# Optimization experiments

Hardware: AMD Instinct MI355X
Metric: run time of the kernel (lower is better)

Reference implementation:

```python
import jax, jax.numpy as jnp
import numpy as np

N_NODES = 50000
N_EDGES = 800000
IN_CH = 128
HID = 64
HEADS = 4
OUT_CH = 12
NEG_SLOPE = 0.2


def setup_inputs() -> dict:
    key = jax.random.key(0)
    ks = jax.random.split(key, 16)
    s = 0.05
    F1 = HEADS * HID  # 256
    return {
        "x": jax.random.normal(ks[0], (N_NODES, IN_CH), jnp.float32),
        "edge_index": jax.random.randint(ks[1], (2, N_EDGES), 0, N_NODES, jnp.int64 if jax.config.jax_enable_x64 else jnp.int32),
        # GAT layer 1 params
        "W1": jax.random.normal(ks[2], (IN_CH, F1), jnp.float32) * s,
        "att_src1": jax.random.normal(ks[3], (HEADS, HID), jnp.float32) * s,
        "att_dst1": jax.random.normal(ks[4], (HEADS, HID), jnp.float32) * s,
        "b1": jnp.zeros((F1,), jnp.float32),
        # GAT layer 2 params
        "W2": jax.random.normal(ks[5], (F1, F1), jnp.float32) * s,
        "att_src2": jax.random.normal(ks[6], (HEADS, HID), jnp.float32) * s,
        "att_dst2": jax.random.normal(ks[7], (HEADS, HID), jnp.float32) * s,
        "b2": jnp.zeros((F1,), jnp.float32),
        # temporal Conv1d(F1 -> HID, k=3, pad=1)
        "conv_w": jax.random.normal(ks[8], (HID, F1, 3), jnp.float32) * s,
        "conv_b": jnp.zeros((HID,), jnp.float32),
        # final Linear(HID -> OUT_CH)
        "lin_w": jax.random.normal(ks[9], (HID, OUT_CH), jnp.float32) * s,
        "lin_b": jnp.zeros((OUT_CH,), jnp.float32),
    }


def _gat_layer(x, src, dst, W, a_src, a_dst, bias):
    # x: [N, Fin]; src/dst: [E] (self-loops already included)
    h = (x @ W).reshape(x.shape[0], HEADS, HID)          # [N, H, C]
    alpha_s = jnp.sum(h * a_src[None], axis=-1)          # [N, H]
    alpha_d = jnp.sum(h * a_dst[None], axis=-1)          # [N, H]
    e = jax.nn.leaky_relu(alpha_s[src] + alpha_d[dst], NEG_SLOPE)  # [E, H]
    # segment softmax over destination nodes
    m = jax.ops.segment_max(e, dst, num_segments=N_NODES)          # [N, H]
    ex = jnp.exp(e - m[dst])
    denom = jax.ops.segment_sum(ex, dst, num_segments=N_NODES)
    alpha = ex / (denom[dst] + 1e-16)                    # [E, H]
    msg = h[src] * alpha[:, :, None]                     # [E, H, C]
    out = jax.ops.segment_sum(msg, dst, num_segments=N_NODES)      # [N, H, C]
    return out.reshape(N_NODES, HEADS * HID) + bias


def reference(x, edge_index, W1, att_src1, att_dst1, b1, W2, att_src2, att_dst2, b2, conv_w, conv_b, lin_w, lin_b):
    # add self loops (PyG GATConv default)
    loops = jnp.arange(N_NODES, dtype=edge_index.dtype)
    src = jnp.concatenate([edge_index[0], loops])
    dst = jnp.concatenate([edge_index[1], loops])

    h = jax.nn.relu(_gat_layer(x, src, dst, W1, att_src1, att_dst1, b1))
    h = jax.nn.relu(_gat_layer(h, src, dst, W2, att_src2, att_dst2, b2))

    # temporal Conv1d over the node axis: [1, F1, N] -> [1, HID, N]
    inp = h.T[None]                                      # [1, F1, N]
    y = jax.lax.conv_general_dilated(inp, conv_w, (1,), [(1, 1)],
                                     dimension_numbers=("NCH", "OIH", "NCH"))
    y = jax.nn.relu(y + conv_b[None, :, None])           # [1, HID, N]
    out = y[0].T @ lin_w + lin_b                         # [N, OUT_CH]
    return out
```

## Files before the change

### kernel.cpp

```cpp
#include <hip/hip_runtime.h>
#include <hip/hip_bf16.h>

#define N_NODES 50000
#define N_EDGES 800000
#define E_TOT   (N_EDGES + N_NODES)
#define IN_CH   128
#define HID     64
#define HEADS   4
#define F1      256
#define OUT_CH  12
#define NEG_SLOPE 0.2f
#define CAP     256

typedef __attribute__((ext_vector_type(8))) short  bf16x8;
typedef __attribute__((ext_vector_type(4))) float  f32x4;

__device__ __forceinline__ float leaky(float x) { return x > 0.f ? x : NEG_SLOPE * x; }

__device__ __forceinline__ unsigned short tob(float f) {
    unsigned u = __float_as_uint(f);
    u += 0x7fffu + ((u >> 16) & 1u);
    return (unsigned short)(u >> 16);
}
__device__ __forceinline__ float fromb(unsigned short s) {
    return __uint_as_float(((unsigned)s) << 16);
}

typedef __attribute__((address_space(3))) unsigned int        lds_u32;
typedef const __attribute__((address_space(1))) unsigned int  glb_u32;
__device__ __forceinline__ void gload16(const void* g, void* l) {
    __builtin_amdgcn_global_load_lds((glb_u32*)g, (lds_u32*)l, 16, 0, 0);
}

__global__ void k_zero(int* p, int n) {
    int i = blockIdx.x * blockDim.x + threadIdx.x;
    if (i < n) p[i] = 0;
}

__global__ void k_guard(unsigned int* front, unsigned int* back) {
    int i = threadIdx.x;
    if (i < 128) front[i] = 0;
    else         back[i - 128] = 0;
}

__global__ void k_count(const int* __restrict__ ei, int* __restrict__ counts) {
    int i = blockIdx.x * blockDim.x + threadIdx.x;
    if (i >= E_TOT) return;
    int dst = (i < N_EDGES) ? ei[N_EDGES + i] : (i - N_EDGES);
    atomicAdd(&counts[dst], 1);
}

__global__ __launch_bounds__(1024) void k_scan(const int* __restrict__ counts,
                                               int* __restrict__ rowptr,
                                               int* __restrict__ cursor) {
    __shared__ int wsum[16];
    __shared__ int carrysh;
    const int lane = threadIdx.x & 63, w = threadIdx.x >> 6;
    if (threadIdx.x == 0) carrysh = 0;
    __syncthreads();
    for (int base = 0; base < N_NODES; base += 1024) {
        int i = base + threadIdx.x;
        int v = (i < N_NODES) ? counts[i] : 0;
        int s = v;
        #pragma unroll
        for (int off = 1; off < 64; off <<= 1) {
            int t = __shfl_up(s, off);
            if (lane >= off) s += t;
        }
        if (lane == 63) wsum[w] = s;
        __syncthreads();
        int woff = 0;
        for (int j = 0; j < w; ++j) woff += wsum[j];
        int incl = carrysh + woff + s;
        if (i < N_NODES) { rowptr[i] = incl - v; cursor[i] = incl - v; }
        __syncthreads();
        if (threadIdx.x == 1023) carrysh = incl;
        __syncthreads();
    }
    if (threadIdx.x == 0) rowptr[N_NODES] = carrysh;
}

__global__ void k_fill(const int* __restrict__ ei, int* __restrict__ cursor,
                       int* __restrict__ csr_src) {
    int i = blockIdx.x * blockDim.x + threadIdx.x;
    if (i >= E_TOT) return;
    int src, dst;
    if (i < N_EDGES) { src = ei[i]; dst = ei[N_EDGES + i]; }
    else             { src = dst = i - N_EDGES; }
    int pos = atomicAdd(&cursor[dst], 1);
    csr_src[pos] = src;
}

__global__ void k_cast4(const float* __restrict__ in, unsigned short* __restrict__ out, int n4) {
    int i = blockIdx.x * blockDim.x + threadIdx.x;
    if (i >= n4) return;
    float4 v = *(const float4*)&in[i * 4];
    ushort4 o;
    o.x = tob(v.x); o.y = tob(v.y); o.z = tob(v.z); o.w = tob(v.w);
    *(ushort4*)&out[i * 4] = o;
}

__global__ void k_prep_wt(const float* __restrict__ W, unsigned short* __restrict__ WT,
                          int K, int N) {
    int idx = blockIdx.x * blockDim.x + threadIdx.x;
    if (idx >= K * N) return;
    int n = idx / K, k = idx % K;
    WT[idx] = tob(W[(size_t)k * N + n]);
}

__global__ void k_prep_cw(const float* __restrict__ CW, unsigned short* __restrict__ BT) {
    int idx = blockIdx.x * blockDim.x + threadIdx.x;
    if (idx >= 64 * 768) return;
    int o = idx / 768, kk = idx % 768;
    int kseg = kk >> 8, c = kk & 255;
    BT[idx] = tob(CW[((size_t)o * 256 + c) * 3 + kseg]);
}

__global__ __launch_bounds__(256) void k_gemm_bf16(const unsigned short* __restrict__ A,
                                                   const unsigned short* __restrict__ BT,
                                                   unsigned short* __restrict__ C,
                                                   int M, int K) {
    __shared__ unsigned short As[128][32];
    __shared__ unsigned short Bs[128][32];
    const int t    = threadIdx.x;
    const int lane = t & 63, wave = t >> 6;
    const int wr = wave >> 1, wc = wave & 1;
    const int row0 = blockIdx.y * 128, col0 = blockIdx.x * 128;
    const int l15 = lane & 15, kg = lane >> 4;

    const int srow = (wave << 4) + (lane >> 2);
    const int sseg = (lane & 3) * 8;
    int ar0 = row0 + srow;      if (ar0 >= M) ar0 = M - 1;
    int ar1 = row0 + srow + 64; if (ar1 >= M) ar1 = M - 1;
    const int br0 = col0 + srow, br1 = col0 + srow + 64;
    unsigned short* ldsA = &As[0][0];
    unsigned short* ldsB = &Bs[0][0];
    const int lofs0 = wave * 512, lofs1 = 2048 + wave * 512;

    f32x4 acc[4][4];
    #pragma unroll
    for (int m = 0; m < 4; ++m)
        #pragma unroll
        for (int n = 0; n < 4; ++n) acc[m][n] = 0.f;

    for (int k0 = 0; k0 < K; k0 += 32) {
        gload16(&A [(size_t)ar0 * K + k0 + sseg], ldsA + lofs0);
        gload16(&A [(size_t)ar1 * K + k0 + sseg], ldsA + lofs1);
        gload16(&BT[(size_t)br0 * K + k0 + sseg], ldsB + lofs0);
        gload16(&BT[(size_t)br1 * K + k0 + sseg], ldsB + lofs1);
        __syncthreads();
        bf16x8 af[4], bf[4];
        #pragma unroll
        for (int m = 0; m < 4; ++m) af[m] = *(const bf16x8*)&As[wr * 64 + m * 16 + l15][kg * 8];
        #pragma unroll
        for (int n = 0; n < 4; ++n) bf[n] = *(const bf16x8*)&Bs[wc * 64 + n * 16 + l15][kg * 8];
        #pragma unroll
        for (int m = 0; m < 4; ++m)
            #pragma unroll
            for (int n = 0; n < 4; ++n)
                acc[m][n] = __builtin_amdgcn_mfma_f32_16x16x32_bf16(af[m], bf[n], acc[m][n], 0, 0, 0);
        __syncthreads();
    }
    #pragma unroll
    for (int m = 0; m < 4; ++m) {
        #pragma unroll
        for (int j = 0; j < 4; ++j) {
            int row = row0 + wr * 64 + m * 16 + (lane >> 4) * 4 + j;
            if (row < M) {
                #pragma unroll
                for (int n = 0; n < 4; ++n)
                    C[(size_t)row * F1 + col0 + wc * 64 + n * 16 + l15] = tob(acc[m][n][j]);
            }
        }
    }
}

__global__ __launch_bounds__(256) void k_attn(const unsigned short* __restrict__ H,
                                              const float* __restrict__ a_src,
                                              const float* __restrict__ a_dst,
                                              float* __restrict__ oS,
                                              float* __restrict__ oD) {
    int lane = threadIdx.x & 63, wid = threadIdx.x >> 6;
    int node = blockIdx.x * 4 + wid;
    int head = lane >> 4, cc = (lane & 15) * 4;
    ushort4 hv4 = *(const ushort4*)&H[(size_t)node * F1 + lane * 4];
    float h0 = fromb(hv4.x), h1 = fromb(hv4.y), h2 = fromb(hv4.z), h3 = fromb(hv4.w);
    float4 sv = *(const float4*)&a_src[head * HID + cc];
    float4 dv = *(const float4*)&a_dst[head * HID + cc];
    float s = h0 * sv.x + h1 * sv.y + h2 * sv.z + h3 * sv.w;
    float d = h0 * dv.x + h1 * dv.y + h2 * dv.z + h3 * dv.w;
    #pragma unroll
    for (int off = 1; off < 16; off <<= 1) {
        s += __shfl_xor(s, off);
        d += __shfl_xor(d, off);
    }
    if ((lane & 15) == 0) { oS[node * 4 + head] = s; oD[node * 4 + head] = d; }
}

__global__ __launch_bounds__(256) void k_agg(const unsigned short* __restrict__ H,
                                             const float* __restrict__ aS,
                                             const float* __restrict__ aD,
                                             const int* __restrict__ rowptr,
                                             const int* __restrict__ csr,
                                             const float* __restrict__ bias,
                                             unsigned short* __restrict__ O) {
    __shared__ float wlds[4][CAP][4];
    int lane = threadIdx.x & 63, wid = threadIdx.x >> 6;
    int node = blockIdx.x * 4 + wid;
    int beg = rowptr[node], end = rowptr[node + 1];
    int deg = end - beg;

    float4 adv = *(const float4*)&aD[node * 4];
    float ad[4] = { adv.x, adv.y, adv.z, adv.w };
    float m[4] = { -1e30f, -1e30f, -1e30f, -1e30f };

    for (int j = beg + lane, idx = lane; j < end; j += 64, idx += 64) {
        int src = csr[j];
        float4 asv = *(const float4*)&aS[src * 4];
        float4 e4;
        e4.x = leaky(asv.x + ad[0]);
        e4.y = leaky(asv.y + ad[1]);
        e4.z = leaky(asv.z + ad[2]);
        e4.w = leaky(asv.w + ad[3]);
        m[0] = fmaxf(m[0], e4.x); m[1] = fmaxf(m[1], e4.y);
        m[2] = fmaxf(m[2], e4.z); m[3] = fmaxf(m[3], e4.w);
        if (idx < CAP) *(float4*)&wlds[wid][idx][0] = e4;
    }
    #pragma unroll
    for (int off = 1; off < 64; off <<= 1) {
        #pragma unroll
        for (int h = 0; h < 4; ++h) m[h] = fmaxf(m[h], __shfl_xor(m[h], off));
    }

    float s[4] = { 0.f, 0.f, 0.f, 0.f };
    int degc = deg < CAP ? deg : CAP;
    for (int idx = lane; idx < degc; idx += 64) {
        float4 e4 = *(float4*)&wlds[wid][idx][0];
        float4 w4;
        w4.x = __expf(e4.x - m[0]); w4.y = __expf(e4.y - m[1]);
        w4.z = __expf(e4.z - m[2]); w4.w = __expf(e4.w - m[3]);
        s[0] += w4.x; s[1] += w4.y; s[2] += w4.z; s[3] += w4.w;
        *(float4*)&wlds[wid][idx][0] = w4;
    }
    for (int j = beg + CAP + lane; j < end; j += 64) {
        int src = csr[j];
        float4 asv = *(const float4*)&aS[src * 4];
        s[0] += __expf(leaky(asv.x + ad[0]) - m[0]);
        s[1] += __expf(leaky(asv.y + ad[1]) - m[1]);
        s[2] += __expf(leaky(asv.z + ad[2]) - m[2]);
        s[3] += __expf(leaky(asv.w + ad[3]) - m[3]);
    }
    #pragma unroll
    for (int off = 1; off < 64; off <<= 1) {
        #pragma unroll
        for (int h = 0; h < 4; ++h) s[h] += __shfl_xor(s[h], off);
    }

    int   hl   = lane >> 4;
    float invh = 1.f / (s[hl] + 1e-16f);
    float mh   = m[hl];
    float adh  = ad[hl];
    float a0 = 0.f, a1 = 0.f, a2 = 0.f, a3 = 0.f;
    for (int idx = 0; idx < degc; ++idx) {
        int src = csr[beg + idx];
        float w = wlds[wid][idx][hl];
        ushort4 hv = *(const ushort4*)&H[(size_t)src * F1 + lane * 4];
        a0 += w * fromb(hv.x); a1 += w * fromb(hv.y);
        a2 += w * fromb(hv.z); a3 += w * fromb(hv.w);
    }
    for (int idx = CAP; idx < deg; ++idx) {
        int src = csr[beg + idx];
        float w = __expf(leaky(aS[src * 4 + hl] + adh) - mh);
        ushort4 hv = *(const ushort4*)&H[(size_t)src * F1 + lane * 4];
        a0 += w * fromb(hv.x); a1 += w * fromb(hv.y);
        a2 += w * fromb(hv.z); a3 += w * fromb(hv.w);
    }
    float4 bv = *(const float4*)&bias[lane * 4];
    ushort4 o;
    o.x = tob(fmaxf(a0 * invh + bv.x, 0.f));
    o.y = tob(fmaxf(a1 * invh + bv.y, 0.f));
    o.z = tob(fmaxf(a2 * invh + bv.z, 0.f));
    o.w = tob(fmaxf(a3 * invh + bv.w, 0.f));
    *(ushort4*)&O[(size_t)node * F1 + lane * 4] = o;
}

__global__ __launch_bounds__(256) void k_conv(const unsigned short* __restrict__ H,
                                              const unsigned short* __restrict__ BcT,
                                              const float* __restrict__ CB,
                                              float* __restrict__ Y) {
    __shared__ unsigned short As[128][32];
    __shared__ unsigned short Bs[64][32];
    const int t    = threadIdx.x;
    const int lane = t & 63, wave = t >> 6;
    const int row0 = blockIdx.x * 128;
    const int l15 = lane & 15, kg = lane >> 4;

    const int srow = (wave << 4) + (lane >> 2);
    const int sseg = (lane & 3) * 8;
    unsigned short* ldsA = &As[0][0];
    unsigned short* ldsB = &Bs[0][0];
    const int lofs0 = wave * 512, lofs1 = 2048 + wave * 512;

    f32x4 acc[2][4];
    #pragma unroll
    for (int m = 0; m < 2; ++m)
        #pragma unroll
        for (int n = 0; n < 4; ++n) acc[m][n] = 0.f;

    for (int k0 = 0; k0 < 768; k0 += 32) {
        int kseg  = k0 >> 8;
        int cbase = (k0 & 255) + sseg;
        int gr0 = row0 + srow + kseg - 1;
        int gr1 = gr0 + 64;
        if (gr1 > N_NODES) gr1 = N_NODES;
        gload16(H + (ptrdiff_t)gr0 * F1 + cbase, ldsA + lofs0);
        gload16(H + (ptrdiff_t)gr1 * F1 + cbase, ldsA + lofs1);
        {
            int brow = srow;
            gload16(&BcT[(size_t)brow * 768 + k0 + sseg], ldsB + lofs0);
        }
        __syncthreads();
        bf16x8 af[2], bf[4];
        #pragma unroll
        for (int m = 0; m < 2; ++m) af[m] = *(const bf16x8*)&As[wave * 32 + m * 16 + l15][kg * 8];
        #pragma unroll
        for (int n = 0; n < 4; ++n) bf[n] = *(const bf16x8*)&Bs[n * 16 + l15][kg * 8];
        #pragma unroll
        for (int m = 0; m < 2; ++m)
            #pragma unroll
            for (int n = 0; n < 4; ++n)
                acc[m][n] = __builtin_amdgcn_mfma_f32_16x16x32_bf16(af[m], bf[n], acc[m][n], 0, 0, 0);
        __syncthreads();
    }
    #pragma unroll
    for (int m = 0; m < 2; ++m) {
        #pragma unroll
        for (int j = 0; j < 4; ++j) {
            int row = row0 + wave * 32 + m * 16 + (lane >> 4) * 4 + j;
            if (row < N_NODES) {
                #pragma unroll
                for (int n = 0; n < 4; ++n) {
                    int col = n * 16 + l15;
                    Y[(size_t)row * HID + col] = fmaxf(acc[m][n][j] + CB[col], 0.f);
                }
            }
        }
    }
}

__global__ __launch_bounds__(256) void k_lin(const float* __restrict__ Y,
                                             const float* __restrict__ LW,
                                             const float* __restrict__ LB,
                                             float* __restrict__ OUT) {
    __shared__ float w[64][12];
    __shared__ float b[12];
    for (int i = threadIdx.x; i < 64 * 12; i += 256) w[i / 12][i % 12] = LW[i];
    if (threadIdx.x < 12) b[threadIdx.x] = LB[threadIdx.x];
    __syncthreads();
    int n = blockIdx.x * 256 + threadIdx.x;
    if (n >= N_NODES) return;
    float acc[12];
    #pragma unroll
    for (int o = 0; o < 12; ++o) acc[o] = b[o];
    for (int c = 0; c < 64; c += 4) {
        float4 yv = *(const float4*)&Y[(size_t)n * HID + c];
        #pragma unroll
        for (int o = 0; o < 12; ++o)
            acc[o] += yv.x * w[c][o] + yv.y * w[c + 1][o]
                    + yv.z * w[c + 2][o] + yv.w * w[c + 3][o];
    }
    #pragma unroll
    for (int o = 0; o < 12; ++o) OUT[(size_t)n * OUT_CH + o] = acc[o];
}

extern "C" void kernel_launch(void* const* d_in, const int* in_sizes, int n_in,
                              void* d_out, int out_size, void* d_ws, size_t ws_size,
                              hipStream_t stream) {
    const float* x   = (const float*)d_in[0];
    const int*   ei  = (const int*)d_in[1];
    const float* W1  = (const float*)d_in[2];
    const float* as1 = (const float*)d_in[3];
    const float* ad1 = (const float*)d_in[4];
    const float* b1  = (const float*)d_in[5];
    const float* W2  = (const float*)d_in[6];
    const float* as2 = (const float*)d_in[7];
    const float* ad2 = (const float*)d_in[8];
    const float* b2  = (const float*)d_in[9];
    const float* cw  = (const float*)d_in[10];
    const float* cb  = (const float*)d_in[11];
    const float* lw  = (const float*)d_in[12];
    const float* lb  = (const float*)d_in[13];
    float* out = (float*)d_out;

    char* ws = (char*)d_ws;
    size_t off = 0;
    auto alloc = [&](size_t bytes) -> void* {
        off = (off + 255) & ~(size_t)255;
        void* p = ws + off;
        off += bytes;
        return p;
    };
    unsigned short* hA  = (unsigned short*)alloc((size_t)N_NODES * F1 * 2);
    unsigned short* hBg = (unsigned short*)alloc((size_t)(N_NODES + 2) * F1 * 2);
    unsigned short* hB  = hBg + F1;
    unsigned short* xb  = (unsigned short*)alloc((size_t)N_NODES * IN_CH * 2);
    unsigned short* wt1 = (unsigned short*)alloc((size_t)F1 * IN_CH * 2);
    unsigned short* wt2 = (unsigned short*)alloc((size_t)F1 * F1 * 2);
    unsigned short* cwt = (unsigned short*)alloc((size_t)HID * 768 * 2);
    float* alS    = (float*)alloc((size_t)N_NODES * 4 * 4);
    float* alD    = (float*)alloc((size_t)N_NODES * 4 * 4);
    int*   counts = (int*)  alloc((size_t)N_NODES * 4);
    int*   rowptr = (int*)  alloc((size_t)(N_NODES + 1) * 4);
    int*   cursor = (int*)  alloc((size_t)N_NODES * 4);
    int*   csr    = (int*)  alloc((size_t)E_TOT * 4);
    float* y      = (float*)alloc((size_t)N_NODES * HID * 4);

    k_zero <<<(N_NODES + 255) / 256, 256, 0, stream>>>(counts, N_NODES);
    k_guard<<<1, 256, 0, stream>>>((unsigned int*)hBg,
                                   (unsigned int*)(hBg + (size_t)(N_NODES + 1) * F1));
    k_count<<<(E_TOT + 255) / 256, 256, 0, stream>>>(ei, counts);
    k_scan <<<1, 1024, 0, stream>>>(counts, rowptr, cursor);
    k_fill <<<(E_TOT + 255) / 256, 256, 0, stream>>>(ei, cursor, csr);

    k_cast4 <<<(N_NODES * IN_CH / 4 + 255) / 256, 256, 0, stream>>>(x, xb, N_NODES * IN_CH / 4);
    k_prep_wt<<<(IN_CH * F1 + 255) / 256, 256, 0, stream>>>(W1, wt1, IN_CH, F1);
    k_prep_wt<<<(F1 * F1 + 255) / 256, 256, 0, stream>>>(W2, wt2, F1, F1);
    k_prep_cw<<<(HID * 768 + 255) / 256, 256, 0, stream>>>(cw, cwt);

    dim3 gg(F1 / 128, (N_NODES + 127) / 128);
    k_gemm_bf16<<<gg, 256, 0, stream>>>(xb, wt1, hA, N_NODES, IN_CH);
    k_attn<<<N_NODES / 4, 256, 0, stream>>>(hA, as1, ad1, alS, alD);
    k_agg <<<N_NODES / 4, 256, 0, stream>>>(hA, alS, alD, rowptr, csr, b1, hB);
    k_gemm_bf16<<<gg, 256, 0, stream>>>(hB, wt2, hA, N_NODES, F1);
    k_attn<<<N_NODES / 4, 256, 0, stream>>>(hA, as2, ad2, alS, alD);
    k_agg <<<N_NODES / 4, 256, 0, stream>>>(hA, alS, alD, rowptr, csr, b2, hB);
    k_conv<<<(N_NODES + 127) / 128, 256, 0, stream>>>(hB, cwt, cb, y);
    k_lin <<<(N_NODES + 255) / 256, 256, 0, stream>>>(y, lw, lb, out);
}
```

Measured before the change: 468.9 us.

## Split GAT aggregation across four edge groups per wave with wide loads

The per-node aggregation used to have all 64 lanes walk every edge serially, each lane holding 4 features. Now the wave is split into four groups of 16 lanes. Each group processes every fourth edge and each lane loads 16 bf16 features with two 128-bit loads. Partial sums are combined with cross-group shuffles and only group 0 writes the output. This raises memory-level parallelism and shortens the serial edge loop, at the cost of more registers, 32 shuffles and idle lanes during the write.

```diff
diff --git a/kernel.cpp b/kernel.cpp
--- a/kernel.cpp
+++ b/kernel.cpp
@@ -256,32 +256,53 @@
         for (int h = 0; h < 4; ++h) s[h] += __shfl_xor(s[h], off);
     }
 
-    int   hl   = lane >> 4;
-    float invh = 1.f / (s[hl] + 1e-16f);
-    float mh   = m[hl];
-    float adh  = ad[hl];
-    float a0 = 0.f, a1 = 0.f, a2 = 0.f, a3 = 0.f;
-    for (int idx = 0; idx < degc; ++idx) {
+    const int g   = lane >> 4;
+    const int l15 = lane & 15;
+    const int hl  = l15 >> 2;
+    float acc[16];
+    #pragma unroll
+    for (int k = 0; k < 16; ++k) acc[k] = 0.f;
+
+    for (int idx = g; idx < degc; idx += 4) {
         int src = csr[beg + idx];
         float w = wlds[wid][idx][hl];
-        ushort4 hv = *(const ushort4*)&H[(size_t)src * F1 + lane * 4];
-        a0 += w * fromb(hv.x); a1 += w * fromb(hv.y);
-        a2 += w * fromb(hv.z); a3 += w * fromb(hv.w);
-    }
-    for (int idx = CAP; idx < deg; ++idx) {
+        const unsigned short* hp = &H[(size_t)src * F1 + l15 * 16];
+        bf16x8 h0 = *(const bf16x8*)hp;
+        bf16x8 h1 = *(const bf16x8*)(hp + 8);
+        #pragma unroll
+        for (int k = 0; k < 8; ++k) acc[k]     += w * fromb((unsigned short)h0[k]);
+        #pragma unroll
+        for (int k = 0; k < 8; ++k) acc[k + 8] += w * fromb((unsigned short)h1[k]);
+    }
+    for (int idx = CAP + g; idx < deg; idx += 4) {
         int src = csr[beg + idx];
-        float w = __expf(leaky(aS[src * 4 + hl] + adh) - mh);
-        ushort4 hv = *(const ushort4*)&H[(size_t)src * F1 + lane * 4];
-        a0 += w * fromb(hv.x); a1 += w * fromb(hv.y);
-        a2 += w * fromb(hv.z); a3 += w * fromb(hv.w);
-    }
-    float4 bv = *(const float4*)&bias[lane * 4];
-    ushort4 o;
-    o.x = tob(fmaxf(a0 * invh + bv.x, 0.f));
-    o.y = tob(fmaxf(a1 * invh + bv.y, 0.f));
-    o.z = tob(fmaxf(a2 * invh + bv.z, 0.f));
-    o.w = tob(fmaxf(a3 * invh + bv.w, 0.f));
-    *(ushort4*)&O[(size_t)node * F1 + lane * 4] = o;
+        float as4[4];
+        *(float4*)as4 = *(const float4*)&aS[src * 4];
+        float w = __expf(leaky(as4[hl] + ad[hl]) - m[hl]);
+        const unsigned short* hp = &H[(size_t)src * F1 + l15 * 16];
+        bf16x8 h0 = *(const bf16x8*)hp;
+        bf16x8 h1 = *(const bf16x8*)(hp + 8);
+        #pragma unroll
+        for (int k = 0; k < 8; ++k) acc[k]     += w * fromb((unsigned short)h0[k]);
+        #pragma unroll
+        for (int k = 0; k < 8; ++k) acc[k + 8] += w * fromb((unsigned short)h1[k]);
+    }
+    #pragma unroll
+    for (int off = 16; off < 64; off <<= 1) {
+        #pragma unroll
+        for (int k = 0; k < 16; ++k) acc[k] += __shfl_xor(acc[k], off);
+    }
+
+    if (g == 0) {
+        float invh = 1.f / (s[hl] + 1e-16f);
+        const float* bp = &bias[l15 * 16];
+        unsigned short ob[16];
+        #pragma unroll
+        for (int k = 0; k < 16; ++k) ob[k] = tob(fmaxf(acc[k] * invh + bp[k], 0.f));
+        unsigned short* op = &O[(size_t)node * F1 + l15 * 16];
+        *(uint4*)op       = *(uint4*)&ob[0];
+        *(uint4*)(op + 8) = *(uint4*)&ob[8];
+    }
 }
 
 __global__ __launch_bounds__(256) void k_conv(const unsigned short* __restrict__ H,
```

Measured after the change: 481.3 us. 2.6% more time.
